# Performance work log

Hardware: AMD Instinct MI355X
Metric: run time of the kernel (lower is better)

Reference implementation:

```python
import jax, jax.numpy as jnp
import numpy as np

N_NODES = 100000
N_EDGES = 1600000

def gcn_conv(x, src, dst, W, b, n):
    # symmetric GCN normalization with self-loops already included in src/dst
    deg = jax.ops.segment_sum(jnp.ones_like(src, dtype=x.dtype), dst, num_segments=n)
    dinv = jnp.where(deg > 0, jax.lax.rsqrt(deg), 0.0)
    norm = dinv[src] * dinv[dst]            # [E]
    h = x @ W                                # [n, out]
    msg = h[src] * norm[:, None]             # gather + scale, [E, out]
    out = jax.ops.segment_sum(msg, dst, num_segments=n)  # scatter-add
    return out + b

def setup_inputs() -> dict:
    key = jax.random.key(0)
    k1, k2, k3, k4 = jax.random.split(key, 4)
    x = jax.random.normal(k1, (N_NODES, 768), dtype=jnp.float32)
    edge_index = jax.random.randint(k2, (2, N_EDGES), 0, N_NODES, dtype=jnp.int64)
    W1 = jax.random.normal(k3, (768, 64), dtype=jnp.float32) * (1.0 / np.sqrt(768))
    b1 = jnp.zeros((64,), dtype=jnp.float32)
    W2 = jax.random.normal(k4, (64, 32), dtype=jnp.float32) * (1.0 / np.sqrt(64))
    b2 = jnp.zeros((32,), dtype=jnp.float32)
    return {"x": x, "edge_index": edge_index, "W1": W1, "b1": b1, "W2": W2, "b2": b2}

def reference(x, edge_index, W1, b1, W2, b2):
    n = x.shape[0]
    loop = jnp.arange(n, dtype=edge_index.dtype)
    src = jnp.concatenate([edge_index[0], loop])
    dst = jnp.concatenate([edge_index[1], loop])
    h = jax.nn.relu(gcn_conv(x, src, dst, W1, b1, n))
    # F.dropout with training=False -> identity (eval mode)
    out = gcn_conv(h, src, dst, W2, b2, n)
    return out
```

## Files before the change

### kernel.cpp

```cpp
#include <hip/hip_runtime.h>


constexpr int C1 = 64;
constexpr int C2 = 32;
constexpr int K1 = 768;
constexpr int SCAN_BS = 256;
constexpr int SCAN_ELEMS = 2048;

typedef __attribute__((ext_vector_type(8))) short short8;
typedef __attribute__((ext_vector_type(4))) float floatx4;

__global__ void detect_k(const int* __restrict__ ei32, int* flag, int n_words) {
    __shared__ int any_nz;
    if (threadIdx.x == 0) any_nz = 0;
    __syncthreads();
    int w = 2 * threadIdx.x + 1;
    if (w < n_words && ei32[w] != 0) atomicOr(&any_nz, 1);
    __syncthreads();
    if (threadIdx.x == 0) *flag = (any_nz == 0) ? 1 : 0;
}

__device__ __forceinline__ int load_idx(const void* ei, size_t pos, int m64) {
    if (m64) return (int)((const long long*)ei)[pos];
    return ((const int*)ei)[pos];
}

__global__ void zero_k(int* p, int n) {
    int i = blockIdx.x * 256 + threadIdx.x;
    if (i < n) p[i] = 0;
}

__global__ void cnt_k(const void* __restrict__ ei, const int* __restrict__ flag,
                      int* cnt, int E) {
    int e = blockIdx.x * 256 + threadIdx.x;
    if (e >= E) return;
    int m64 = *flag;
    int d = load_idx(ei, (size_t)E + e, m64);
    atomicAdd(&cnt[d], 1);
}

__global__ void dinv_k(const int* __restrict__ cnt, float* dinv, int n) {
    int i = blockIdx.x * 256 + threadIdx.x;
    if (i < n) dinv[i] = rsqrtf(1.0f + (float)cnt[i]);
}

__global__ void scan1_k(const int* __restrict__ cnt, int* partials, int n) {
    __shared__ int s[SCAN_BS];
    int base = blockIdx.x * SCAN_ELEMS;
    int t = threadIdx.x;
    int sum = 0;
    #pragma unroll
    for (int i = 0; i < 8; ++i) {
        int idx = base + t * 8 + i;
        if (idx < n) sum += cnt[idx];
    }
    s[t] = sum;
    __syncthreads();
    for (int off = 128; off > 0; off >>= 1) {
        if (t < off) s[t] += s[t + off];
        __syncthreads();
    }
    if (t == 0) partials[blockIdx.x] = s[0];
}

__global__ void scan2_k(int* partials, int* total_out, int nb) {
    __shared__ int s[256];
    int t = threadIdx.x;
    int v = (t < nb) ? partials[t] : 0;
    s[t] = v;
    __syncthreads();
    for (int off = 1; off < 256; off <<= 1) {
        int add = (t >= off) ? s[t - off] : 0;
        __syncthreads();
        s[t] += add;
        __syncthreads();
    }
    if (t < nb) partials[t] = s[t] - v;
    if (t == 0) *total_out = s[255];
}

__global__ void scan3_k(const int* __restrict__ cnt, const int* __restrict__ partials,
                        int* offsets, int* cursor, int n) {
    __shared__ int s[SCAN_BS];
    int base = blockIdx.x * SCAN_ELEMS;
    int t = threadIdx.x;
    int local[8];
    int sum = 0;
    #pragma unroll
    for (int i = 0; i < 8; ++i) {
        int idx = base + t * 8 + i;
        int v = (idx < n) ? cnt[idx] : 0;
        local[i] = sum;
        sum += v;
    }
    int mine = sum;
    s[t] = sum;
    __syncthreads();
    for (int off = 1; off < 256; off <<= 1) {
        int add = (t >= off) ? s[t - off] : 0;
        __syncthreads();
        s[t] += add;
        __syncthreads();
    }
    int texcl = s[t] - mine;
    int boff = partials[blockIdx.x];
    #pragma unroll
    for (int i = 0; i < 8; ++i) {
        int idx = base + t * 8 + i;
        if (idx < n) {
            int o = boff + texcl + local[i];
            offsets[idx] = o;
            cursor[idx] = o;
        }
    }
}

__global__ void fill_k(const void* __restrict__ ei, const int* __restrict__ flag,
                       int* cursor, int* adj, int E) {
    int e = blockIdx.x * 256 + threadIdx.x;
    if (e >= E) return;
    int m64 = *flag;
    int s = load_idx(ei, e, m64);
    int d = load_idx(ei, (size_t)E + e, m64);
    int pos = atomicAdd(&cursor[d], 1);
    adj[pos] = s;
}

__device__ __forceinline__ void bf16_split(float f, short& hi, short& lo) {
    unsigned int u = __float_as_uint(f);
    unsigned int r = u + (0x7FFFu + ((u >> 16) & 1u));
    hi = (short)(r >> 16);
    float rem = f - __uint_as_float(r & 0xFFFF0000u);
    lo = (short)(__float_as_uint(rem) >> 16);
}

__device__ __forceinline__ void split8(const float4& a, const float4& b,
                                       short8& h, short8& v) {
    float f[8] = {a.x, a.y, a.z, a.w, b.x, b.y, b.z, b.w};
    #pragma unroll
    for (int j = 0; j < 8; ++j) {
        short hh, ll;
        bf16_split(f[j], hh, ll);
        h[j] = hh;
        v[j] = ll;
    }
}

__global__ void packW1_k(const float* __restrict__ W1, unsigned short* __restrict__ Bp) {
    int gid = blockIdx.x * 256 + threadIdx.x;
    if (gid >= 24 * 4 * 2 * 64) return;
    int l    = gid & 63;
    int frag = gid >> 6;
    int p = frag & 1;
    int t = (frag >> 1) & 3;
    int s = frag >> 3;
    int c = t * 16 + (l & 15);
    int kbase = s * 32 + (l >> 4) * 8;
    short8 v;
    #pragma unroll
    for (int j = 0; j < 8; ++j) {
        short hi, lo;
        bf16_split(W1[(size_t)(kbase + j) * C1 + c], hi, lo);
        v[j] = p ? lo : hi;
    }
    *(short8*)(Bp + (size_t)gid * 8) = v;
}

__global__ __launch_bounds__(256, 3) void gemm1_k(const float* __restrict__ x,
                                                  const unsigned short* __restrict__ Bp,
                                                  const float* __restrict__ dinv,
                                                  float* __restrict__ g1, int n) {
    const int tid = threadIdx.x;
    const int w = tid >> 6;
    const int l = tid & 63;
    const int block_row = blockIdx.x * 128;
    const int wrow = block_row + w * 32;

    int row0 = wrow + (l & 15);        if (row0 > n - 1) row0 = n - 1;
    int row1 = wrow + 16 + (l & 15);   if (row1 > n - 1) row1 = n - 1;
    const int kl = (l >> 4) * 8;

    const float* __restrict__ pa0 = x + (size_t)row0 * K1 + kl;
    const float* __restrict__ pa1 = x + (size_t)row1 * K1 + kl;
    const unsigned short* __restrict__ pb = Bp + l * 8;

    floatx4 zero = {0.f, 0.f, 0.f, 0.f};
    floatx4 acc[2][4];
    #pragma unroll
    for (int r = 0; r < 2; ++r)
        #pragma unroll
        for (int t = 0; t < 4; ++t) acc[r][t] = zero;

    float4 a0a = *(const float4*)(pa0 + 0);
    float4 a0b = *(const float4*)(pa0 + 4);
    float4 a1a = *(const float4*)(pa1 + 0);
    float4 a1b = *(const float4*)(pa1 + 4);

    for (int t = 0; t < 24; ++t) {
        const int tn = (t + 1 < 24) ? (t + 1) * 32 : 0;
        float4 n0a = *(const float4*)(pa0 + tn);
        float4 n0b = *(const float4*)(pa0 + tn + 4);
        float4 n1a = *(const float4*)(pa1 + tn);
        float4 n1b = *(const float4*)(pa1 + tn + 4);

        const unsigned short* bt = pb + t * 4096;
        short8 bh[4], bl[4];
        #pragma unroll
        for (int tt = 0; tt < 4; ++tt) {
            bh[tt] = *(const short8*)(bt + (tt * 2 + 0) * 512);
            bl[tt] = *(const short8*)(bt + (tt * 2 + 1) * 512);
        }

        short8 ah0, al0, ah1, al1;
        split8(a0a, a0b, ah0, al0);
        split8(a1a, a1b, ah1, al1);

        #pragma unroll
        for (int tt = 0; tt < 4; ++tt) {
            acc[0][tt] = __builtin_amdgcn_mfma_f32_16x16x32_bf16(ah0, bl[tt], acc[0][tt], 0, 0, 0);
            acc[0][tt] = __builtin_amdgcn_mfma_f32_16x16x32_bf16(al0, bh[tt], acc[0][tt], 0, 0, 0);
            acc[0][tt] = __builtin_amdgcn_mfma_f32_16x16x32_bf16(ah0, bh[tt], acc[0][tt], 0, 0, 0);
            acc[1][tt] = __builtin_amdgcn_mfma_f32_16x16x32_bf16(ah1, bl[tt], acc[1][tt], 0, 0, 0);
            acc[1][tt] = __builtin_amdgcn_mfma_f32_16x16x32_bf16(al1, bh[tt], acc[1][tt], 0, 0, 0);
            acc[1][tt] = __builtin_amdgcn_mfma_f32_16x16x32_bf16(ah1, bh[tt], acc[1][tt], 0, 0, 0);
        }

        a0a = n0a; a0b = n0b; a1a = n1a; a1b = n1b;
    }

    #pragma unroll
    for (int r = 0; r < 2; ++r) {
        #pragma unroll
        for (int i = 0; i < 4; ++i) {
            int row = block_row + w * 32 + r * 16 + (l >> 4) * 4 + i;
            if (row < n) {
                float dv = dinv[row];
                #pragma unroll
                for (int t = 0; t < 4; ++t) {
                    g1[(size_t)row * C1 + t * 16 + (l & 15)] = acc[r][t][i] * dv;
                }
            }
        }
    }
}

__global__ __launch_bounds__(256) void gather1_k(const int* __restrict__ offsets,
                                                 const int* __restrict__ adj,
                                                 const float* __restrict__ dinv,
                                                 const float* __restrict__ g1,
                                                 const float* __restrict__ b1,
                                                 const float* __restrict__ W2,
                                                 float* __restrict__ g2, int n) {
    __shared__ float sW[C1 * C2];
    __shared__ float srow[4][C1];
    const int tid = threadIdx.x;
    for (int i = tid; i < C1 * C2; i += 256) sW[i] = W2[i];

    const int wid = tid >> 6;
    const int c = tid & 63;
    const int v = blockIdx.x * 4 + wid;

    float r = 0.f;
    float dv = 0.f;
    if (v < n) {
        dv = dinv[v];
        int start = offsets[v], end = offsets[v + 1];
        float acc = g1[(size_t)v * C1 + c];
        int j = start;
        for (; j + 4 <= end; j += 4) {
            int s0 = adj[j], s1 = adj[j + 1], s2 = adj[j + 2], s3 = adj[j + 3];
            float a0 = g1[(size_t)s0 * C1 + c];
            float a1 = g1[(size_t)s1 * C1 + c];
            float a2 = g1[(size_t)s2 * C1 + c];
            float a3 = g1[(size_t)s3 * C1 + c];
            acc += (a0 + a1) + (a2 + a3);
        }
        for (; j < end; ++j) acc += g1[(size_t)adj[j] * C1 + c];
        r = fmaxf(b1[c] + dv * acc, 0.f);
    }
    srow[wid][c] = r;
    __syncthreads();

    if (v < n && c < C2) {
        float acc = 0.f;
        #pragma unroll
        for (int k = 0; k < C1; ++k) acc += srow[wid][k] * sW[k * C2 + c];
        g2[(size_t)v * C2 + c] = dv * acc;
    }
}

__global__ __launch_bounds__(256) void gather2_k(const int* __restrict__ offsets,
                                                 const int* __restrict__ adj,
                                                 const float* __restrict__ dinv,
                                                 const float* __restrict__ g2,
                                                 const float* __restrict__ b2,
                                                 float* __restrict__ out, int n) {
    int v = blockIdx.x * 8 + (threadIdx.x >> 5);
    int c = threadIdx.x & 31;
    if (v >= n) return;
    int start = offsets[v], end = offsets[v + 1];
    float acc = g2[(size_t)v * C2 + c];
    int j = start;
    for (; j + 4 <= end; j += 4) {
        int s0 = adj[j], s1 = adj[j + 1], s2 = adj[j + 2], s3 = adj[j + 3];
        float a0 = g2[(size_t)s0 * C2 + c];
        float a1 = g2[(size_t)s1 * C2 + c];
        float a2 = g2[(size_t)s2 * C2 + c];
        float a3 = g2[(size_t)s3 * C2 + c];
        acc += (a0 + a1) + (a2 + a3);
    }
    for (; j < end; ++j) acc += g2[(size_t)adj[j] * C2 + c];
    out[(size_t)v * C2 + c] = b2[c] + dinv[v] * acc;
}

extern "C" void kernel_launch(void* const* d_in, const int* in_sizes, int n_in,
                              void* d_out, int out_size, void* d_ws, size_t ws_size,
                              hipStream_t stream) {
    const float* x  = (const float*)d_in[0];
    const void*  ei = d_in[1];
    const float* W1 = (const float*)d_in[2];
    const float* b1 = (const float*)d_in[3];
    const float* W2 = (const float*)d_in[4];
    const float* b2 = (const float*)d_in[5];
    float* out = (float*)d_out;

    const int n = in_sizes[0] / K1;
    const int E = in_sizes[1] / 2;

    float* ws      = (float*)d_ws;
    int*   flag    = (int*)ws;
    float* dinv    = ws + 16;
    float* g1      = dinv + n;
    float* g2      = g1 + (size_t)n * C1;
    int*   cnt     = (int*)(g2 + (size_t)n * C2);
    int*   offsets = cnt + n;
    int*   cursor  = offsets + n + 1;
    int*   partials= cursor + n;
    int*   adj     = partials + 256;
    uintptr_t bp_a = ((uintptr_t)(adj + E) + 15) & ~(uintptr_t)15;
    unsigned short* Bp = (unsigned short*)bp_a;

    const int nb_scan = (n + SCAN_ELEMS - 1) / SCAN_ELEMS;

    detect_k<<<1, 256, 0, stream>>>((const int*)ei, flag, in_sizes[1]);
    zero_k<<<(n + 255) / 256, 256, 0, stream>>>(cnt, n);
    cnt_k<<<(E + 255) / 256, 256, 0, stream>>>(ei, flag, cnt, E);
    dinv_k<<<(n + 255) / 256, 256, 0, stream>>>(cnt, dinv, n);

    packW1_k<<<48, 256, 0, stream>>>(W1, Bp);
    gemm1_k<<<(n + 127) / 128, 256, 0, stream>>>(x, Bp, dinv, g1, n);

    scan1_k<<<nb_scan, SCAN_BS, 0, stream>>>(cnt, partials, n);
    scan2_k<<<1, 256, 0, stream>>>(partials, offsets + n, nb_scan);
    scan3_k<<<nb_scan, SCAN_BS, 0, stream>>>(cnt, partials, offsets, cursor, n);
    fill_k<<<(E + 255) / 256, 256, 0, stream>>>(ei, flag, cursor, adj, E);

    gather1_k<<<(n + 3) / 4, 256, 0, stream>>>(offsets, adj, dinv, g1, b1, W2, g2, n);
    gather2_k<<<(n + 7) / 8, 256, 0, stream>>>(offsets, adj, dinv, g2, b2, out, n);
}
```

Baseline: 818.8 us.

## Vectorize CSR gathers to float4 per lane and double-step GEMM prefetch

Both neighbor-aggregation kernels now have each lane load a float4 of a neighbor row instead of one float. This packs 4 nodes per wavefront in layer 1 and 8 in layer 2, with proportionally fewer blocks. The goal is fewer memory instructions and more independent row gathers in flight, which matters because these gathers are latency-bound. The layer-1 GEMM loop is also unrolled to cover two K-tiles per iteration with a deeper A prefetch. The cost is more registers per thread, which could lower occupancy.

Result: faster. 791.9 us (-3.3%).

```diff
diff --git a/kernel.cpp b/kernel.cpp
--- a/kernel.cpp
+++ b/kernel.cpp
@@ -191,41 +191,70 @@
         #pragma unroll
         for (int t = 0; t < 4; ++t) acc[r][t] = zero;
 
-    float4 a0a = *(const float4*)(pa0 + 0);
-    float4 a0b = *(const float4*)(pa0 + 4);
-    float4 a1a = *(const float4*)(pa1 + 0);
-    float4 a1b = *(const float4*)(pa1 + 4);
-
-    for (int t = 0; t < 24; ++t) {
-        const int tn = (t + 1 < 24) ? (t + 1) * 32 : 0;
-        float4 n0a = *(const float4*)(pa0 + tn);
-        float4 n0b = *(const float4*)(pa0 + tn + 4);
-        float4 n1a = *(const float4*)(pa1 + tn);
-        float4 n1b = *(const float4*)(pa1 + tn + 4);
-
-        const unsigned short* bt = pb + t * 4096;
+    float4 c00 = *(const float4*)(pa0 + 0);
+    float4 c01 = *(const float4*)(pa0 + 4);
+    float4 c02 = *(const float4*)(pa0 + 32);
+    float4 c03 = *(const float4*)(pa0 + 36);
+    float4 c10 = *(const float4*)(pa1 + 0);
+    float4 c11 = *(const float4*)(pa1 + 4);
+    float4 c12 = *(const float4*)(pa1 + 32);
+    float4 c13 = *(const float4*)(pa1 + 36);
+
+    for (int t = 0; t < 12; ++t) {
+        const int kn = (t + 1 < 12) ? (t + 1) * 64 : 0;
+        float4 m00 = *(const float4*)(pa0 + kn + 0);
+        float4 m01 = *(const float4*)(pa0 + kn + 4);
+        float4 m02 = *(const float4*)(pa0 + kn + 32);
+        float4 m03 = *(const float4*)(pa0 + kn + 36);
+        float4 m10 = *(const float4*)(pa1 + kn + 0);
+        float4 m11 = *(const float4*)(pa1 + kn + 4);
+        float4 m12 = *(const float4*)(pa1 + kn + 32);
+        float4 m13 = *(const float4*)(pa1 + kn + 36);
+
         short8 bh[4], bl[4];
-        #pragma unroll
-        for (int tt = 0; tt < 4; ++tt) {
-            bh[tt] = *(const short8*)(bt + (tt * 2 + 0) * 512);
-            bl[tt] = *(const short8*)(bt + (tt * 2 + 1) * 512);
-        }
-
         short8 ah0, al0, ah1, al1;
-        split8(a0a, a0b, ah0, al0);
-        split8(a1a, a1b, ah1, al1);
-
-        #pragma unroll
-        for (int tt = 0; tt < 4; ++tt) {
-            acc[0][tt] = __builtin_amdgcn_mfma_f32_16x16x32_bf16(ah0, bl[tt], acc[0][tt], 0, 0, 0);
-            acc[0][tt] = __builtin_amdgcn_mfma_f32_16x16x32_bf16(al0, bh[tt], acc[0][tt], 0, 0, 0);
-            acc[0][tt] = __builtin_amdgcn_mfma_f32_16x16x32_bf16(ah0, bh[tt], acc[0][tt], 0, 0, 0);
-            acc[1][tt] = __builtin_amdgcn_mfma_f32_16x16x32_bf16(ah1, bl[tt], acc[1][tt], 0, 0, 0);
-            acc[1][tt] = __builtin_amdgcn_mfma_f32_16x16x32_bf16(al1, bh[tt], acc[1][tt], 0, 0, 0);
-            acc[1][tt] = __builtin_amdgcn_mfma_f32_16x16x32_bf16(ah1, bh[tt], acc[1][tt], 0, 0, 0);
-        }
-
-        a0a = n0a; a0b = n0b; a1a = n1a; a1b = n1b;
+
+        {
+            const unsigned short* bt = pb + (size_t)(2 * t) * 4096;
+            #pragma unroll
+            for (int tt = 0; tt < 4; ++tt) {
+                bh[tt] = *(const short8*)(bt + (tt * 2 + 0) * 512);
+                bl[tt] = *(const short8*)(bt + (tt * 2 + 1) * 512);
+            }
+            split8(c00, c01, ah0, al0);
+            split8(c10, c11, ah1, al1);
+            #pragma unroll
+            for (int tt = 0; tt < 4; ++tt) {
+                acc[0][tt] = __builtin_amdgcn_mfma_f32_16x16x32_bf16(ah0, bl[tt], acc[0][tt], 0, 0, 0);
+                acc[0][tt] = __builtin_amdgcn_mfma_f32_16x16x32_bf16(al0, bh[tt], acc[0][tt], 0, 0, 0);
+                acc[0][tt] = __builtin_amdgcn_mfma_f32_16x16x32_bf16(ah0, bh[tt], acc[0][tt], 0, 0, 0);
+                acc[1][tt] = __builtin_amdgcn_mfma_f32_16x16x32_bf16(ah1, bl[tt], acc[1][tt], 0, 0, 0);
+                acc[1][tt] = __builtin_amdgcn_mfma_f32_16x16x32_bf16(al1, bh[tt], acc[1][tt], 0, 0, 0);
+                acc[1][tt] = __builtin_amdgcn_mfma_f32_16x16x32_bf16(ah1, bh[tt], acc[1][tt], 0, 0, 0);
+            }
+        }
+        {
+            const unsigned short* bt = pb + (size_t)(2 * t + 1) * 4096;
+            #pragma unroll
+            for (int tt = 0; tt < 4; ++tt) {
+                bh[tt] = *(const short8*)(bt + (tt * 2 + 0) * 512);
+                bl[tt] = *(const short8*)(bt + (tt * 2 + 1) * 512);
+            }
+            split8(c02, c03, ah0, al0);
+            split8(c12, c13, ah1, al1);
+            #pragma unroll
+            for (int tt = 0; tt < 4; ++tt) {
+                acc[0][tt] = __builtin_amdgcn_mfma_f32_16x16x32_bf16(ah0, bl[tt], acc[0][tt], 0, 0, 0);
+                acc[0][tt] = __builtin_amdgcn_mfma_f32_16x16x32_bf16(al0, bh[tt], acc[0][tt], 0, 0, 0);
+                acc[0][tt] = __builtin_amdgcn_mfma_f32_16x16x32_bf16(ah0, bh[tt], acc[0][tt], 0, 0, 0);
+                acc[1][tt] = __builtin_amdgcn_mfma_f32_16x16x32_bf16(ah1, bl[tt], acc[1][tt], 0, 0, 0);
+                acc[1][tt] = __builtin_amdgcn_mfma_f32_16x16x32_bf16(al1, bh[tt], acc[1][tt], 0, 0, 0);
+                acc[1][tt] = __builtin_amdgcn_mfma_f32_16x16x32_bf16(ah1, bh[tt], acc[1][tt], 0, 0, 0);
+            }
+        }
+
+        c00 = m00; c01 = m01; c02 = m02; c03 = m03;
+        c10 = m10; c11 = m11; c12 = m12; c13 = m13;
     }
 
     #pragma unroll
@@ -252,40 +281,65 @@
                                                  const float* __restrict__ W2,
                                                  float* __restrict__ g2, int n) {
     __shared__ float sW[C1 * C2];
-    __shared__ float srow[4][C1];
+    __shared__ float srow[16][C1];
+    __shared__ float sdv[16];
     const int tid = threadIdx.x;
     for (int i = tid; i < C1 * C2; i += 256) sW[i] = W2[i];
 
-    const int wid = tid >> 6;
-    const int c = tid & 63;
-    const int v = blockIdx.x * 4 + wid;
-
-    float r = 0.f;
+    const int wid  = tid >> 6;
+    const int l    = tid & 63;
+    const int grp  = l >> 4;
+    const int lc   = l & 15;
+    const int slot = wid * 4 + grp;
+    const int v    = blockIdx.x * 16 + slot;
+    const int c0   = lc * 4;
+
+    float4 acc = make_float4(0.f, 0.f, 0.f, 0.f);
     float dv = 0.f;
     if (v < n) {
         dv = dinv[v];
+        acc = *(const float4*)(g1 + (size_t)v * C1 + c0);
         int start = offsets[v], end = offsets[v + 1];
-        float acc = g1[(size_t)v * C1 + c];
         int j = start;
         for (; j + 4 <= end; j += 4) {
             int s0 = adj[j], s1 = adj[j + 1], s2 = adj[j + 2], s3 = adj[j + 3];
-            float a0 = g1[(size_t)s0 * C1 + c];
-            float a1 = g1[(size_t)s1 * C1 + c];
-            float a2 = g1[(size_t)s2 * C1 + c];
-            float a3 = g1[(size_t)s3 * C1 + c];
-            acc += (a0 + a1) + (a2 + a3);
-        }
-        for (; j < end; ++j) acc += g1[(size_t)adj[j] * C1 + c];
-        r = fmaxf(b1[c] + dv * acc, 0.f);
-    }
-    srow[wid][c] = r;
-    __syncthreads();
-
-    if (v < n && c < C2) {
-        float acc = 0.f;
-        #pragma unroll
-        for (int k = 0; k < C1; ++k) acc += srow[wid][k] * sW[k * C2 + c];
-        g2[(size_t)v * C2 + c] = dv * acc;
+            float4 a0 = *(const float4*)(g1 + (size_t)s0 * C1 + c0);
+            float4 a1 = *(const float4*)(g1 + (size_t)s1 * C1 + c0);
+            float4 a2 = *(const float4*)(g1 + (size_t)s2 * C1 + c0);
+            float4 a3 = *(const float4*)(g1 + (size_t)s3 * C1 + c0);
+            acc.x += (a0.x + a1.x) + (a2.x + a3.x);
+            acc.y += (a0.y + a1.y) + (a2.y + a3.y);
+            acc.z += (a0.z + a1.z) + (a2.z + a3.z);
+            acc.w += (a0.w + a1.w) + (a2.w + a3.w);
+        }
+        for (; j < end; ++j) {
+            float4 a = *(const float4*)(g1 + (size_t)adj[j] * C1 + c0);
+            acc.x += a.x; acc.y += a.y; acc.z += a.z; acc.w += a.w;
+        }
+        float4 bb = *(const float4*)(b1 + c0);
+        acc.x = fmaxf(bb.x + dv * acc.x, 0.f);
+        acc.y = fmaxf(bb.y + dv * acc.y, 0.f);
+        acc.z = fmaxf(bb.z + dv * acc.z, 0.f);
+        acc.w = fmaxf(bb.w + dv * acc.w, 0.f);
+    }
+    srow[slot][c0 + 0] = acc.x;
+    srow[slot][c0 + 1] = acc.y;
+    srow[slot][c0 + 2] = acc.z;
+    srow[slot][c0 + 3] = acc.w;
+    if (lc == 0) sdv[slot] = dv;
+    __syncthreads();
+
+    #pragma unroll
+    for (int rep = 0; rep < 2; ++rep) {
+        int node = (tid >> 5) + rep * 8;
+        int c = tid & 31;
+        int vv = blockIdx.x * 16 + node;
+        if (vv < n) {
+            float a = 0.f;
+            #pragma unroll
+            for (int k = 0; k < C1; ++k) a += srow[node][k] * sW[k * C2 + c];
+            g2[(size_t)vv * C2 + c] = sdv[node] * a;
+        }
     }
 }
 
@@ -295,22 +349,38 @@
                                                  const float* __restrict__ g2,
                                                  const float* __restrict__ b2,
                                                  float* __restrict__ out, int n) {
-    int v = blockIdx.x * 8 + (threadIdx.x >> 5);
-    int c = threadIdx.x & 31;
+    const int tid = threadIdx.x;
+    const int wid = tid >> 6;
+    const int l   = tid & 63;
+    const int grp = l >> 3;
+    const int lc  = l & 7;
+    const int v   = blockIdx.x * 32 + wid * 8 + grp;
+    const int c0  = lc * 4;
     if (v >= n) return;
+
+    float4 acc = *(const float4*)(g2 + (size_t)v * C2 + c0);
     int start = offsets[v], end = offsets[v + 1];
-    float acc = g2[(size_t)v * C2 + c];
     int j = start;
     for (; j + 4 <= end; j += 4) {
         int s0 = adj[j], s1 = adj[j + 1], s2 = adj[j + 2], s3 = adj[j + 3];
-        float a0 = g2[(size_t)s0 * C2 + c];
-        float a1 = g2[(size_t)s1 * C2 + c];
-        float a2 = g2[(size_t)s2 * C2 + c];
-        float a3 = g2[(size_t)s3 * C2 + c];
-        acc += (a0 + a1) + (a2 + a3);
-    }
-    for (; j < end; ++j) acc += g2[(size_t)adj[j] * C2 + c];
-    out[(size_t)v * C2 + c] = b2[c] + dinv[v] * acc;
+        float4 a0 = *(const float4*)(g2 + (size_t)s0 * C2 + c0);
+        float4 a1 = *(const float4*)(g2 + (size_t)s1 * C2 + c0);
+        float4 a2 = *(const float4*)(g2 + (size_t)s2 * C2 + c0);
+        float4 a3 = *(const float4*)(g2 + (size_t)s3 * C2 + c0);
+        acc.x += (a0.x + a1.x) + (a2.x + a3.x);
+        acc.y += (a0.y + a1.y) + (a2.y + a3.y);
+        acc.z += (a0.z + a1.z) + (a2.z + a3.z);
+        acc.w += (a0.w + a1.w) + (a2.w + a3.w);
+    }
+    for (; j < end; ++j) {
+        float4 a = *(const float4*)(g2 + (size_t)adj[j] * C2 + c0);
+        acc.x += a.x; acc.y += a.y; acc.z += a.z; acc.w += a.w;
+    }
+    float dv = dinv[v];
+    float4 bb = *(const float4*)(b2 + c0);
+    float4 o = make_float4(bb.x + dv * acc.x, bb.y + dv * acc.y,
+                           bb.z + dv * acc.z, bb.w + dv * acc.w);
+    *(float4*)(out + (size_t)v * C2 + c0) = o;
 }
 
 extern "C" void kernel_launch(void* const* d_in, const int* in_sizes, int n_in,
@@ -355,6 +425,6 @@
     scan3_k<<<nb_scan, SCAN_BS, 0, stream>>>(cnt, partials, offsets, cursor, n);
     fill_k<<<(E + 255) / 256, 256, 0, stream>>>(ei, flag, cursor, adj, E);
 
-    gather1_k<<<(n + 3) / 4, 256, 0, stream>>>(offsets, adj, dinv, g1, b1, W2, g2, n);
-    gather2_k<<<(n + 7) / 8, 256, 0, stream>>>(offsets, adj, dinv, g2, b2, out, n);
-}
+    gather1_k<<<(n + 15) / 16, 256, 0, stream>>>(offsets, adj, dinv, g1, b1, W2, g2, n);
+    gather2_k<<<(n + 31) / 32, 256, 0, stream>>>(offsets, adj, dinv, g2, b2, out, n);
+}
```
